# Performance work log

Measured on AMD Instinct MI355X. Metric: run time of the kernel, lower is better.

## Reference

```python
import jax, jax.numpy as jnp
import numpy as np

BS, N, DIM, HEADS = 4, 2048, 512, 8
HEAD_DIM = DIM // HEADS
SCALE = HEAD_DIM ** 0.5
NEG = -1000000.0


def setup_inputs() -> dict:
    key = jax.random.key(0)
    ks = jax.random.split(key, 6)
    x = jax.random.normal(ks[0], (BS, N, DIM), dtype=jnp.float32)
    mask = jax.random.randint(ks[1], (BS, N), 0, 2, dtype=jnp.int32)
    s = 1.0 / np.sqrt(DIM)
    Wq = jax.random.normal(ks[2], (DIM, DIM), dtype=jnp.float32) * s
    Wk = jax.random.normal(ks[3], (DIM, DIM), dtype=jnp.float32) * s
    Wv = jax.random.normal(ks[4], (DIM, DIM), dtype=jnp.float32) * s
    Wo = jax.random.normal(ks[5], (DIM, DIM), dtype=jnp.float32) * s
    return {"x": x, "Wq": Wq, "Wk": Wk, "Wv": Wv, "Wo": Wo, "mask": mask}


def reference(x, Wq, Wk, Wv, Wo, mask):
    # q,k,v: (bs, n, dim) -> (bs, h, n, d)
    def split_heads(t):
        return t.reshape(BS, N, HEADS, HEAD_DIM).transpose(0, 2, 1, 3)
    q = split_heads(x @ Wq.T)
    k = split_heads(x @ Wk.T)
    v = split_heads(x @ Wv.T)
    # scores: (bs, h, n, n)
    scores = jnp.einsum('bhqd,bhkd->bhqk', q, k) / SCALE
    # key-padding mask broadcast over heads and query positions
    keep = (mask == 1)[:, None, None, :]  # (bs,1,1,n)
    scores = jnp.where(keep, scores, NEG)
    attn = jax.nn.softmax(scores, axis=-1)
    out = jnp.einsum('bhqk,bhkd->bhqd', attn, v)
    out = out.transpose(0, 2, 1, 3).reshape(BS, N, DIM)
    return out @ Wo.T
```

## Files before the change

kernel.cpp:

```cpp
#include <hip/hip_runtime.h>
#include <hip/hip_bf16.h>

#define BS 4
#define SEQ 2048
#define DIM 512
#define HEADS 8
#define HD 64
#define ROWS (BS*SEQ)
#define SCL2E 0.1803368801111244f
#define NEGB (-1.4426950408889634e6f)

typedef __attribute__((ext_vector_type(8))) short bf16x8;
typedef __attribute__((ext_vector_type(4))) short bf16x4;
typedef __attribute__((ext_vector_type(4))) float floatx4;
typedef unsigned short u16;
typedef unsigned int u32;

#if defined(__has_builtin)
# if __has_builtin(__builtin_amdgcn_mfma_f32_16x16x16bf16_1k)
#  define HAVE_MFMA16 1
# endif
#endif
#ifndef HAVE_MFMA16
# define HAVE_MFMA16 0
#endif

__device__ __forceinline__ u16 f2bf(float f) {
    union { float f; unsigned u; } v; v.f = f;
    unsigned r = v.u + 0x7fff + ((v.u >> 16) & 1);
    return (u16)(r >> 16);
}

__device__ __forceinline__ unsigned pack2bf(float a, float b) {
#if __has_builtin(__builtin_amdgcn_cvt_pk_bf16_f32)
    typedef __attribute__((ext_vector_type(2))) __bf16 bf2;
    union { bf2 v; unsigned u; } cv;
    cv.v = __builtin_amdgcn_cvt_pk_bf16_f32(a, b);
    return cv.u;
#else
    return (unsigned)f2bf(a) | ((unsigned)f2bf(b) << 16);
#endif
}

__device__ __forceinline__ float fexp2(float x) {
#if __has_builtin(__builtin_amdgcn_exp2f)
    return __builtin_amdgcn_exp2f(x);
#else
    return __expf(x * 0.6931471805599453f);
#endif
}

__device__ __forceinline__ void gload16(const u16* g, u16* l) {
    __builtin_amdgcn_global_load_lds(
        (const __attribute__((address_space(1))) u32*)g,
        (__attribute__((address_space(3))) u32*)l, 16, 0, 0);
}

__global__ __launch_bounds__(256) void convert_all(
    const float* __restrict__ x, const float* __restrict__ Wq,
    const float* __restrict__ Wk, const float* __restrict__ Wv,
    const float* __restrict__ Wo, const int* __restrict__ mask,
    u16* __restrict__ xb, u16* __restrict__ wqb,
    u16* __restrict__ wkb, u16* __restrict__ wvb,
    u16* __restrict__ wob, float* __restrict__ biasf)
{
    int i = blockIdx.x * 256 + threadIdx.x;
    if (i < 1048576 + 262144) {
        const float* src; u16* dst; int off;
        if (i < 1048576) { src = x; dst = xb; off = i; }
        else {
            int j = i - 1048576; int seg = j >> 16; off = j & 65535;
            src = seg == 0 ? Wq : seg == 1 ? Wk : seg == 2 ? Wv : Wo;
            dst = seg == 0 ? wqb : seg == 1 ? wkb : seg == 2 ? wvb : wob;
        }
        float4 v = ((const float4*)src)[off];
        ushort4 o;
        o.x = f2bf(v.x); o.y = f2bf(v.y); o.z = f2bf(v.z); o.w = f2bf(v.w);
        ((ushort4*)dst)[off] = o;
    } else {
        int jb = i - 1310720;
        int4 mv = ((const int4*)mask)[jb];
        float4 bo;
        bo.x = (mv.x == 1) ? 0.f : NEGB;
        bo.y = (mv.y == 1) ? 0.f : NEGB;
        bo.z = (mv.z == 1) ? 0.f : NEGB;
        bo.w = (mv.w == 1) ? 0.f : NEGB;
        ((float4*)biasf)[jb] = bo;
    }
}

__global__ __launch_bounds__(256, 3) void gemm_qkv_fused(
    const u16* __restrict__ A, const u16* __restrict__ Wcat,
    u16* __restrict__ Oq, u16* __restrict__ Okf, u16* __restrict__ Ovf)
{
    __shared__ u16 ldsA[8192];
    __shared__ u16 ldsB[8192];

    int n0 = blockIdx.x * 128;
    int m0 = blockIdx.y * 128;
    int tid = threadIdx.x;
    int w = tid >> 6, lane = tid & 63, quad = lane >> 4, l16 = lane & 15;
    int mo = (w & 1) * 64, no = (w >> 1) * 64;
    int l7 = l16 & 7;

    int sr = lane >> 3, sc = lane & 7, gc = sc ^ sr;
    const u16* gA0 = A    + (long)(m0 + sr) * DIM + gc * 8;
    const u16* gB0 = Wcat + (long)(n0 + sr) * DIM + gc * 8;

    floatx4 acc[4][4];
    #pragma unroll
    for (int mt = 0; mt < 4; mt++)
        #pragma unroll
        for (int nt = 0; nt < 4; nt++) acc[mt][nt] = (floatx4){0.f,0.f,0.f,0.f};

    for (int k0 = 0; k0 < DIM; k0 += 64) {
        #pragma unroll
        for (int i = 0; i < 4; i++) {
            int ch = w * 4 + i;
            gload16(gA0 + (long)ch * 8 * DIM + k0, &ldsA[ch * 512]);
            gload16(gB0 + (long)ch * 8 * DIM + k0, &ldsB[ch * 512]);
        }
        __syncthreads();

        #pragma unroll
        for (int kc = 0; kc < 2; kc++) {
            int swz = ((kc * 4 + quad) ^ l7) * 8;
            bf16x8 af[4], bf[4];
            #pragma unroll
            for (int t4 = 0; t4 < 4; t4++) {
                af[t4] = *(const bf16x8*)&ldsA[(mo + t4*16 + l16) * 64 + swz];
                bf[t4] = *(const bf16x8*)&ldsB[(no + t4*16 + l16) * 64 + swz];
            }
            #pragma unroll
            for (int mt = 0; mt < 4; mt++)
                #pragma unroll
                for (int nt = 0; nt < 4; nt++)
                    acc[mt][nt] = __builtin_amdgcn_mfma_f32_16x16x32_bf16(
                        af[mt], bf[nt], acc[mt][nt], 0, 0, 0);
        }
        __syncthreads();
    }

    int seg = n0 >> 9;
    if (seg == 0) {
        #pragma unroll
        for (int mt = 0; mt < 4; mt++)
            #pragma unroll
            for (int nt = 0; nt < 4; nt++)
                #pragma unroll
                for (int r = 0; r < 4; r++) {
                    int row = m0 + mo + mt*16 + quad*4 + r;
                    int col9 = (n0 + no + nt*16 + l16) & 511;
                    int b = row >> 11, n = row & 2047, h = col9 >> 6, d = col9 & 63;
                    Oq[(((long)(b * HEADS + h) * SEQ + n) << 6) + d] = f2bf(acc[mt][nt][r]);
                }
    } else if (seg == 1) {
        #pragma unroll
        for (int mt = 0; mt < 4; mt++)
            #pragma unroll
            for (int nt = 0; nt < 4; nt++)
                #pragma unroll
                for (int r = 0; r < 4; r++) {
                    int row = m0 + mo + mt*16 + quad*4 + r;
                    int col9 = (n0 + no + nt*16 + l16) & 511;
                    int b = row >> 11, keyn = row & 2047, h = col9 >> 6, dd = col9 & 63;
                    int kt = keyn >> 6, ntk = (keyn >> 4) & 3, l16k = keyn & 15;
                    int g = dd >> 5, quadk = (dd >> 3) & 3, j = dd & 7;
                    long offv = ((long)((b*HEADS + h)*32 + kt) << 12)
                              + ((ntk*2 + g) << 9) + ((quadk*16 + l16k) << 3) + j;
                    Okf[offv] = f2bf(acc[mt][nt][r] * SCL2E);
                }
    } else {
#if HAVE_MFMA16
        #pragma unroll
        for (int mt = 0; mt < 4; mt++)
            #pragma unroll
            for (int nt = 0; nt < 4; nt++) {
                int rowb = m0 + mo + mt*16 + quad*4;
                int col9 = (n0 + no + nt*16 + l16) & 511;
                int b = rowb >> 11, keyn = rowb & 2047, h = col9 >> 6, dd = col9 & 63;
                int kt = keyn >> 6;
                int klo16 = mt;
                int ctv = dd >> 4, d15 = dd & 15;
                long offv = ((long)((b*HEADS + h)*32 + kt) << 12)
                          + ((klo16*4 + ctv) << 8) + ((quad*16 + d15) << 2);
                ushort4 st;
                st.x = f2bf(acc[mt][nt][0]); st.y = f2bf(acc[mt][nt][1]);
                st.z = f2bf(acc[mt][nt][2]); st.w = f2bf(acc[mt][nt][3]);
                *(ushort4*)&Ovf[offv] = st;
            }
#else
        #pragma unroll
        for (int mt = 0; mt < 4; mt++)
            #pragma unroll
            for (int nt = 0; nt < 4; nt++) {
                int rowb = m0 + mo + mt*16 + quad*4;
                int col9 = (n0 + no + nt*16 + l16) & 511;
                int b = rowb >> 11, keyn = rowb & 2047, h = col9 >> 6, dd = col9 & 63;
                int kt = keyn >> 6, g = (keyn >> 5) & 1, quadv = (keyn >> 3) & 3, jk = keyn & 7;
                int ctv = dd >> 4, l16v = dd & 15;
                long offv = ((long)((b*HEADS + h)*32 + kt) << 12)
                          + ((ctv*2 + g) << 9) + ((quadv*16 + l16v) << 3) + jk;
                ushort4 st;
                st.x = f2bf(acc[mt][nt][0]); st.y = f2bf(acc[mt][nt][1]);
                st.z = f2bf(acc[mt][nt][2]); st.w = f2bf(acc[mt][nt][3]);
                *(ushort4*)&Ovf[offv] = st;
            }
#endif
    }
}

#if HAVE_MFMA16
__global__ __launch_bounds__(256, 3) void flash_attn(
    const u16* __restrict__ Q, const u16* __restrict__ Kf,
    const u16* __restrict__ Vf, const float* __restrict__ biasf,
    u16* __restrict__ ctx)
{
    __shared__ u16 lds[16384];

    int bx = blockIdx.x;
    int q0 = (bx & 31) * 64;
    int h  = (bx >> 5) & 7;
    int b  = bx >> 8;
    int bh = b * HEADS + h;

    int tid = threadIdx.x;
    int w = tid >> 6, lane = tid & 63, quad = lane >> 4, l16 = lane & 15;

    bf16x8 qb[4][2];
    #pragma unroll
    for (int nt = 0; nt < 4; nt++) {
        const u16* qp = Q + ((long)bh * SEQ + q0 + nt*16 + l16) * HD + quad * 8;
        qb[nt][0] = *(const bf16x8*)(qp);
        qb[nt][1] = *(const bf16x8*)(qp + 32);
    }

    const u16* Kbh = Kf + ((long)bh << 17);
    const u16* Vbh = Vf + ((long)bh << 17);
    const float* bb = biasf + b * SEQ + w*16 + quad*4;

    u16* K0 = &lds[0];    u16* K1 = &lds[4096];
    u16* V0 = &lds[8192]; u16* V1 = &lds[12288];

    gload16(Kbh + w*1024       + lane*8, K0 + w*1024);
    gload16(Kbh + w*1024 + 512 + lane*8, K0 + w*1024 + 512);
    gload16(Vbh + w*1024       + lane*8, V0 + w*1024);
    gload16(Vbh + w*1024 + 512 + lane*8, V0 + w*1024 + 512);

    floatx4 o[4][4];
    #pragma unroll
    for (int nt = 0; nt < 4; nt++)
        #pragma unroll
        for (int ct = 0; ct < 4; ct++) o[nt][ct] = (floatx4){0.f,0.f,0.f,0.f};
    float ls[4] = {0.f, 0.f, 0.f, 0.f};

    for (int t = 0; t < 32; t++) {
        u16* Kc = (t & 1) ? K1 : K0;
        u16* Vc = (t & 1) ? V1 : V0;
        u16* Kn = (t & 1) ? K0 : K1;
        u16* Vn = (t & 1) ? V0 : V1;

        __builtin_amdgcn_s_waitcnt(0x0F70);

        bf16x8 ka0 = *(const bf16x8*)(Kc + w*1024       + lane*8);
        bf16x8 ka1 = *(const bf16x8*)(Kc + w*1024 + 512 + lane*8);
        bf16x4 vb[4];
        #pragma unroll
        for (int ct = 0; ct < 4; ct++)
            vb[ct] = *(const bf16x4*)(Vc + w*1024 + ct*256 + lane*4);

        if (t < 31) {
            const u16* kp = Kbh + (long)(t+1)*4096 + w*1024 + lane*8;
            const u16* vp = Vbh + (long)(t+1)*4096 + w*1024 + lane*8;
            gload16(kp,       Kn + w*1024);
            gload16(kp + 512, Kn + w*1024 + 512);
            gload16(vp,       Vn + w*1024);
            gload16(vp + 512, Vn + w*1024 + 512);
        }

        float4 bv = *(const float4*)(bb + t*64);

        #pragma unroll
        for (int nt = 0; nt < 4; nt++) {
            floatx4 s;
            s[0] = bv.x; s[1] = bv.y; s[2] = bv.z; s[3] = bv.w;
            s = __builtin_amdgcn_mfma_f32_16x16x32_bf16(ka0, qb[nt][0], s, 0, 0, 0);
            s = __builtin_amdgcn_mfma_f32_16x16x32_bf16(ka1, qb[nt][1], s, 0, 0, 0);
            float p0 = fexp2(s[0]);
            float p1 = fexp2(s[1]);
            float p2 = fexp2(s[2]);
            float p3 = fexp2(s[3]);
            ls[nt] += (p0 + p1) + (p2 + p3);
            union { bf16x4 v; unsigned u[2]; } pu;
            pu.u[0] = pack2bf(p0, p1);
            pu.u[1] = pack2bf(p2, p3);
            #pragma unroll
            for (int ct = 0; ct < 4; ct++)
                o[nt][ct] = __builtin_amdgcn_mfma_f32_16x16x16bf16_1k(
                    pu.v, vb[ct], o[nt][ct], 0, 0, 0);
        }
    }

    __syncthreads();
    float* ldsf = (float*)lds;
    floatx4* ldsv = (floatx4*)lds;

    #pragma unroll
    for (int nt = 0; nt < 4; nt++) {
        ls[nt] += __shfl_xor(ls[nt], 16);
        ls[nt] += __shfl_xor(ls[nt], 32);
    }
    if (quad == 0) {
        #pragma unroll
        for (int nt = 0; nt < 4; nt++)
            ldsf[4096 + w*64 + nt*16 + l16] = ls[nt];
    }
    __syncthreads();

    #pragma unroll
    for (int i = 1; i < 4; i++) {
        int tslot = (w + i) & 3;
        #pragma unroll
        for (int nt = 0; nt < 4; nt++)
            if (nt == tslot) {
                #pragma unroll
                for (int ct = 0; ct < 4; ct++)
                    ldsv[nt*256 + ct*64 + lane] = o[nt][ct];
            }
        __syncthreads();
        #pragma unroll
        for (int nt = 0; nt < 4; nt++)
            if (nt == w) {
                #pragma unroll
                for (int ct = 0; ct < 4; ct++) {
                    floatx4 v = ldsv[nt*256 + ct*64 + lane];
                    o[nt][ct] += v;
                }
            }
        __syncthreads();
    }

    #pragma unroll
    for (int nt = 0; nt < 4; nt++) {
        if (nt != w) continue;
        float inv[4];
        #pragma unroll
        for (int r = 0; r < 4; r++) {
            int q = w*16 + quad*4 + r;
            float s = ldsf[4096 + q] + ldsf[4096 + 64 + q]
                    + ldsf[4096 + 128 + q] + ldsf[4096 + 192 + q];
            inv[r] = 1.0f / s;
        }
        #pragma unroll
        for (int ct = 0; ct < 4; ct++) {
            int col = h * HD + ct*16 + l16;
            long rb = (long)(b * SEQ + q0 + w*16 + quad*4);
            #pragma unroll
            for (int r = 0; r < 4; r++)
                ctx[(rb + r) * DIM + col] = f2bf(o[nt][ct][r] * inv[r]);
        }
    }
}
#else
__global__ __launch_bounds__(256, 4) void flash_attn(
    const u16* __restrict__ Q, const u16* __restrict__ Kf,
    const u16* __restrict__ Vf, const float* __restrict__ biasf,
    u16* __restrict__ ctx)
{
    __shared__ u16 lds[20480];

    int bx = blockIdx.x;
    int q0 = (bx & 31) * 64;
    int h  = (bx >> 5) & 7;
    int b  = bx >> 8;
    int bh = b * HEADS + h;

    int tid = threadIdx.x;
    int w = tid >> 6, lane = tid & 63, quad = lane >> 4, l16 = lane & 15;

    const u16* Qp = Q + ((long)bh * SEQ + q0 + w*16 + l16) * HD + quad * 8;
    bf16x8 qb0 = *(const bf16x8*)(Qp);
    bf16x8 qb1 = *(const bf16x8*)(Qp + 32);

    const u16* Kbh = Kf + ((long)bh << 17);
    const u16* Vbh = Vf + ((long)bh << 17);
    const float* bbase = biasf + b * SEQ + quad * 4;

    u16* Prow = &lds[16384 + w * 1024 + l16 * 64];
    int swz = l16 & 7;

    {
        const u16* gk = Kbh + (2*w)*512 + lane*8;
        const u16* gv = Vbh + (2*w)*512 + lane*8;
        gload16(gk,       &lds[(2*w)*512]);
        gload16(gk + 512, &lds[(2*w+1)*512]);
        gload16(gv,       &lds[8192 + (2*w)*512]);
        gload16(gv + 512, &lds[8192 + (2*w+1)*512]);
    }
    __syncthreads();

    floatx4 o[4];
    #pragma unroll
    for (int ct = 0; ct < 4; ct++) o[ct] = (floatx4){0.f, 0.f, 0.f, 0.f};
    float lsum = 0.f;

    for (int t = 0; t < 32; t++) {
        int cur = t & 1;
        if (t < 31) {
            long tb = (long)(t + 1) << 12;
            int nb = cur ^ 1;
            const u16* gk = Kbh + tb + (2*w)*512 + lane*8;
            const u16* gv = Vbh + tb + (2*w)*512 + lane*8;
            gload16(gk,       &lds[nb*4096 + (2*w)*512]);
            gload16(gk + 512, &lds[nb*4096 + (2*w+1)*512]);
            gload16(gv,       &lds[8192 + nb*4096 + (2*w)*512]);
            gload16(gv + 512, &lds[8192 + nb*4096 + (2*w+1)*512]);
        }

        const u16* Kl = &lds[cur * 4096];
        const u16* Vl = &lds[8192 + cur * 4096];

        #pragma unroll
        for (int nt = 0; nt < 4; nt++) {
            float4 bv = *(const float4*)(bbase + t*64 + nt*16);
            bf16x8 ka0 = *(const bf16x8*)(Kl + (nt*2 + 0)*512 + lane*8);
            bf16x8 ka1 = *(const bf16x8*)(Kl + (nt*2 + 1)*512 + lane*8);
            floatx4 tt;
            tt[0] = bv.x; tt[1] = bv.y; tt[2] = bv.z; tt[3] = bv.w;
            tt = __builtin_amdgcn_mfma_f32_16x16x32_bf16(ka0, qb0, tt, 0, 0, 0);
            tt = __builtin_amdgcn_mfma_f32_16x16x32_bf16(ka1, qb1, tt, 0, 0, 0);
            float p0 = fexp2(tt[0]);
            float p1 = fexp2(tt[1]);
            float p2 = fexp2(tt[2]);
            float p3 = fexp2(tt[3]);
            lsum += (p0 + p1) + (p2 + p3);
            int gx = nt*2 + (quad >> 1);
            uint2 pu;
            pu.x = pack2bf(p0, p1);
            pu.y = pack2bf(p2, p3);
            *(uint2*)(Prow + ((gx ^ swz) << 3) + (quad & 1)*4) = pu;
        }

        #pragma unroll
        for (int g = 0; g < 2; g++) {
            bf16x8 pa = *(const bf16x8*)(Prow + (((g*4 + quad) ^ swz) << 3));
            #pragma unroll
            for (int ct = 0; ct < 4; ct++) {
                bf16x8 vbf = *(const bf16x8*)(Vl + (ct*2 + g)*512 + lane*8);
                o[ct] = __builtin_amdgcn_mfma_f32_16x16x32_bf16(pa, vbf, o[ct], 0, 0, 0);
            }
        }

        __syncthreads();
    }

    lsum += __shfl_xor(lsum, 16);
    lsum += __shfl_xor(lsum, 32);
    float inv = 1.0f / lsum;
    float i0 = __shfl(inv, quad*4 + 0);
    float i1 = __shfl(inv, quad*4 + 1);
    float i2 = __shfl(inv, quad*4 + 2);
    float i3 = __shfl(inv, quad*4 + 3);
    #pragma unroll
    for (int ct = 0; ct < 4; ct++) {
        int col = h * HD + ct*16 + l16;
        long rb = (long)(b * SEQ + q0 + w*16 + quad*4);
        ctx[(rb + 0) * DIM + col] = f2bf(o[ct][0] * i0);
        ctx[(rb + 1) * DIM + col] = f2bf(o[ct][1] * i1);
        ctx[(rb + 2) * DIM + col] = f2bf(o[ct][2] * i2);
        ctx[(rb + 3) * DIM + col] = f2bf(o[ct][3] * i3);
    }
}
#endif

__global__ __launch_bounds__(256, 3) void gemm_proj(
    const u16* __restrict__ A, const u16* __restrict__ Bt,
    float* __restrict__ Out)
{
    __shared__ u16 ldsA[8192];
    __shared__ u16 ldsB[8192];

    int n0 = blockIdx.x * 128;
    int m0 = blockIdx.y * 128;
    int tid = threadIdx.x;
    int w = tid >> 6, lane = tid & 63, quad = lane >> 4, l16 = lane & 15;
    int mo = (w & 1) * 64, no = (w >> 1) * 64;
    int l7 = l16 & 7;

    int sr = lane >> 3, sc = lane & 7, gc = sc ^ sr;
    const u16* gA0 = A  + (long)(m0 + sr) * DIM + gc * 8;
    const u16* gB0 = Bt + (long)(n0 + sr) * DIM + gc * 8;

    floatx4 acc[4][4];
    #pragma unroll
    for (int mt = 0; mt < 4; mt++)
        #pragma unroll
        for (int nt = 0; nt < 4; nt++) acc[mt][nt] = (floatx4){0.f,0.f,0.f,0.f};

    for (int k0 = 0; k0 < DIM; k0 += 64) {
        #pragma unroll
        for (int i = 0; i < 4; i++) {
            int ch = w * 4 + i;
            gload16(gA0 + (long)ch * 8 * DIM + k0, &ldsA[ch * 512]);
            gload16(gB0 + (long)ch * 8 * DIM + k0, &ldsB[ch * 512]);
        }
        __syncthreads();

        #pragma unroll
        for (int kc = 0; kc < 2; kc++) {
            int swz = ((kc * 4 + quad) ^ l7) * 8;
            bf16x8 af[4], bf[4];
            #pragma unroll
            for (int t4 = 0; t4 < 4; t4++) {
                af[t4] = *(const bf16x8*)&ldsA[(mo + t4*16 + l16) * 64 + swz];
                bf[t4] = *(const bf16x8*)&ldsB[(no + t4*16 + l16) * 64 + swz];
            }
            #pragma unroll
            for (int mt = 0; mt < 4; mt++)
                #pragma unroll
                for (int nt = 0; nt < 4; nt++)
                    acc[mt][nt] = __builtin_amdgcn_mfma_f32_16x16x32_bf16(
                        af[mt], bf[nt], acc[mt][nt], 0, 0, 0);
        }
        __syncthreads();
    }

    #pragma unroll
    for (int mt = 0; mt < 4; mt++)
        #pragma unroll
        for (int nt = 0; nt < 4; nt++)
            #pragma unroll
            for (int r = 0; r < 4; r++) {
                int row = m0 + mo + mt*16 + quad*4 + r;
                int col = n0 + no + nt*16 + l16;
                Out[(long)row * DIM + col] = acc[mt][nt][r];
            }
}

extern "C" void kernel_launch(void* const* d_in, const int* in_sizes, int n_in,
                              void* d_out, int out_size, void* d_ws, size_t ws_size,
                              hipStream_t stream) {
    const float* x  = (const float*)d_in[0];
    const float* Wq = (const float*)d_in[1];
    const float* Wk = (const float*)d_in[2];
    const float* Wv = (const float*)d_in[3];
    const float* Wo = (const float*)d_in[4];
    const int* mask = (const int*)d_in[5];
    float* out = (float*)d_out;

    char* ws = (char*)d_ws;
    size_t off = 0;
    u16* xb  = (u16*)(ws + off); off += (size_t)ROWS * DIM * 2;
    u16* wqb = (u16*)(ws + off); off += (size_t)DIM * DIM * 2;
    u16* wkb = (u16*)(ws + off); off += (size_t)DIM * DIM * 2;
    u16* wvb = (u16*)(ws + off); off += (size_t)DIM * DIM * 2;
    u16* wob = (u16*)(ws + off); off += (size_t)DIM * DIM * 2;
    u16* Qh  = (u16*)(ws + off); off += (size_t)ROWS * DIM * 2;
    u16* Kfr = (u16*)(ws + off); off += (size_t)ROWS * DIM * 2;
    u16* Vfr = (u16*)(ws + off); off += (size_t)ROWS * DIM * 2;
    u16* ctx = (u16*)(ws + off); off += (size_t)ROWS * DIM * 2;
    float* biasf = (float*)(ws + off); off += (size_t)BS * SEQ * 4;

    convert_all<<<5128, 256, 0, stream>>>(x, Wq, Wk, Wv, Wo, mask,
                                          xb, wqb, wkb, wvb, wob, biasf);
    gemm_qkv_fused<<<dim3(12, 64), 256, 0, stream>>>(xb, wqb, Qh, Kfr, Vfr);
    flash_attn<<<BS * HEADS * (SEQ / 64), 256, 0, stream>>>(Qh, Kfr, Vfr, biasf, ctx);
    gemm_proj<<<dim3(4, 64), 256, 0, stream>>>(ctx, wob, out);

    (void)in_sizes; (void)n_in; (void)out_size; (void)ws_size;
}
```

Before: 173.5 us.

## Load K/V fragments directly to registers in attention and shrink projection tiles

Measured after the change: 164.3 us. 5.3% less time.

```diff
diff --git a/kernel.cpp b/kernel.cpp
--- a/kernel.cpp
+++ b/kernel.cpp
@@ -180,10 +180,10 @@
                 int col9 = (n0 + no + nt*16 + l16) & 511;
                 int b = rowb >> 11, keyn = rowb & 2047, h = col9 >> 6, dd = col9 & 63;
                 int kt = keyn >> 6;
-                int klo16 = mt;
-                int ctv = dd >> 4, d15 = dd & 15;
+                int wf = (keyn >> 4) & 3, quadf = (keyn >> 2) & 3;
+                int ctf = dd >> 4, l16f = dd & 15;
                 long offv = ((long)((b*HEADS + h)*32 + kt) << 12)
-                          + ((klo16*4 + ctv) << 8) + ((quad*16 + d15) << 2);
+                          + (wf << 10) + ((quadf*16 + l16f) << 4) + (ctf << 2);
                 ushort4 st;
                 st.x = f2bf(acc[mt][nt][0]); st.y = f2bf(acc[mt][nt][1]);
                 st.z = f2bf(acc[mt][nt][2]); st.w = f2bf(acc[mt][nt][3]);
@@ -216,7 +216,7 @@
     const u16* __restrict__ Vf, const float* __restrict__ biasf,
     u16* __restrict__ ctx)
 {
-    __shared__ u16 lds[16384];
+    __shared__ float red[4352];
 
     int bx = blockIdx.x;
     int q0 = (bx & 31) * 64;
@@ -235,17 +235,15 @@
         qb[nt][1] = *(const bf16x8*)(qp + 32);
     }
 
-    const u16* Kbh = Kf + ((long)bh << 17);
-    const u16* Vbh = Vf + ((long)bh << 17);
+    const u16* Kbh = Kf + ((long)bh << 17) + w*1024 + lane*8;
+    const u16* Vbh = Vf + ((long)bh << 17) + w*1024 + lane*16;
     const float* bb = biasf + b * SEQ + w*16 + quad*4;
 
-    u16* K0 = &lds[0];    u16* K1 = &lds[4096];
-    u16* V0 = &lds[8192]; u16* V1 = &lds[12288];
-
-    gload16(Kbh + w*1024       + lane*8, K0 + w*1024);
-    gload16(Kbh + w*1024 + 512 + lane*8, K0 + w*1024 + 512);
-    gload16(Vbh + w*1024       + lane*8, V0 + w*1024);
-    gload16(Vbh + w*1024 + 512 + lane*8, V0 + w*1024 + 512);
+    bf16x8 ka0 = *(const bf16x8*)(Kbh);
+    bf16x8 ka1 = *(const bf16x8*)(Kbh + 512);
+    bf16x8 vlo = *(const bf16x8*)(Vbh);
+    bf16x8 vhi = *(const bf16x8*)(Vbh + 8);
+    float4 bv  = *(const float4*)(bb);
 
     floatx4 o[4][4];
     #pragma unroll
@@ -254,31 +252,23 @@
         for (int ct = 0; ct < 4; ct++) o[nt][ct] = (floatx4){0.f,0.f,0.f,0.f};
     float ls[4] = {0.f, 0.f, 0.f, 0.f};
 
+    #pragma unroll 2
     for (int t = 0; t < 32; t++) {
-        u16* Kc = (t & 1) ? K1 : K0;
-        u16* Vc = (t & 1) ? V1 : V0;
-        u16* Kn = (t & 1) ? K0 : K1;
-        u16* Vn = (t & 1) ? V0 : V1;
-
-        __builtin_amdgcn_s_waitcnt(0x0F70);
-
-        bf16x8 ka0 = *(const bf16x8*)(Kc + w*1024       + lane*8);
-        bf16x8 ka1 = *(const bf16x8*)(Kc + w*1024 + 512 + lane*8);
-        bf16x4 vb[4];
-        #pragma unroll
-        for (int ct = 0; ct < 4; ct++)
-            vb[ct] = *(const bf16x4*)(Vc + w*1024 + ct*256 + lane*4);
-
+        bf16x8 ka0n = ka0, ka1n = ka1, vlon = vlo, vhin = vhi;
+        float4 bvn = bv;
         if (t < 31) {
-            const u16* kp = Kbh + (long)(t+1)*4096 + w*1024 + lane*8;
-            const u16* vp = Vbh + (long)(t+1)*4096 + w*1024 + lane*8;
-            gload16(kp,       Kn + w*1024);
-            gload16(kp + 512, Kn + w*1024 + 512);
-            gload16(vp,       Vn + w*1024);
-            gload16(vp + 512, Vn + w*1024 + 512);
-        }
-
-        float4 bv = *(const float4*)(bb + t*64);
+            const u16* kp = Kbh + (long)(t+1)*4096;
+            const u16* vp = Vbh + (long)(t+1)*4096;
+            ka0n = *(const bf16x8*)(kp);
+            ka1n = *(const bf16x8*)(kp + 512);
+            vlon = *(const bf16x8*)(vp);
+            vhin = *(const bf16x8*)(vp + 8);
+            bvn  = *(const float4*)(bb + (t+1)*64);
+        }
+
+        union { bf16x8 v8; bf16x4 v4[2]; } uvl, uvh;
+        uvl.v8 = vlo; uvh.v8 = vhi;
+        bf16x4 vb[4] = { uvl.v4[0], uvl.v4[1], uvh.v4[0], uvh.v4[1] };
 
         #pragma unroll
         for (int nt = 0; nt < 4; nt++) {
@@ -299,11 +289,13 @@
                 o[nt][ct] = __builtin_amdgcn_mfma_f32_16x16x16bf16_1k(
                     pu.v, vb[ct], o[nt][ct], 0, 0, 0);
         }
+
+        ka0 = ka0n; ka1 = ka1n; vlo = vlon; vhi = vhin; bv = bvn;
     }
 
     __syncthreads();
-    float* ldsf = (float*)lds;
-    floatx4* ldsv = (floatx4*)lds;
+    float* ldsf = red;
+    floatx4* ldsv = (floatx4*)red;
 
     #pragma unroll
     for (int nt = 0; nt < 4; nt++) {
@@ -473,68 +465,57 @@
 }
 #endif
 
-__global__ __launch_bounds__(256, 3) void gemm_proj(
+__global__ __launch_bounds__(256, 4) void gemm_proj(
     const u16* __restrict__ A, const u16* __restrict__ Bt,
     float* __restrict__ Out)
 {
-    __shared__ u16 ldsA[8192];
+    __shared__ u16 ldsA[4096];
     __shared__ u16 ldsB[8192];
 
     int n0 = blockIdx.x * 128;
-    int m0 = blockIdx.y * 128;
+    int m0 = blockIdx.y * 64;
     int tid = threadIdx.x;
     int w = tid >> 6, lane = tid & 63, quad = lane >> 4, l16 = lane & 15;
-    int mo = (w & 1) * 64, no = (w >> 1) * 64;
     int l7 = l16 & 7;
 
     int sr = lane >> 3, sc = lane & 7, gc = sc ^ sr;
     const u16* gA0 = A  + (long)(m0 + sr) * DIM + gc * 8;
     const u16* gB0 = Bt + (long)(n0 + sr) * DIM + gc * 8;
 
-    floatx4 acc[4][4];
-    #pragma unroll
-    for (int mt = 0; mt < 4; mt++)
-        #pragma unroll
-        for (int nt = 0; nt < 4; nt++) acc[mt][nt] = (floatx4){0.f,0.f,0.f,0.f};
+    floatx4 acc[8];
+    #pragma unroll
+    for (int nt = 0; nt < 8; nt++) acc[nt] = (floatx4){0.f,0.f,0.f,0.f};
 
     for (int k0 = 0; k0 < DIM; k0 += 64) {
-        #pragma unroll
-        for (int i = 0; i < 4; i++) {
-            int ch = w * 4 + i;
-            gload16(gA0 + (long)ch * 8 * DIM + k0, &ldsA[ch * 512]);
-            gload16(gB0 + (long)ch * 8 * DIM + k0, &ldsB[ch * 512]);
-        }
+        gload16(gA0 + (long)(2*w)   * 8 * DIM + k0, &ldsA[(2*w)   * 512]);
+        gload16(gA0 + (long)(2*w+1) * 8 * DIM + k0, &ldsA[(2*w+1) * 512]);
+        #pragma unroll
+        for (int i = 0; i < 4; i++)
+            gload16(gB0 + (long)(4*w+i) * 8 * DIM + k0, &ldsB[(4*w+i) * 512]);
         __syncthreads();
 
         #pragma unroll
         for (int kc = 0; kc < 2; kc++) {
             int swz = ((kc * 4 + quad) ^ l7) * 8;
-            bf16x8 af[4], bf[4];
-            #pragma unroll
-            for (int t4 = 0; t4 < 4; t4++) {
-                af[t4] = *(const bf16x8*)&ldsA[(mo + t4*16 + l16) * 64 + swz];
-                bf[t4] = *(const bf16x8*)&ldsB[(no + t4*16 + l16) * 64 + swz];
-            }
-            #pragma unroll
-            for (int mt = 0; mt < 4; mt++)
-                #pragma unroll
-                for (int nt = 0; nt < 4; nt++)
-                    acc[mt][nt] = __builtin_amdgcn_mfma_f32_16x16x32_bf16(
-                        af[mt], bf[nt], acc[mt][nt], 0, 0, 0);
-        }
-        __syncthreads();
-    }
-
-    #pragma unroll
-    for (int mt = 0; mt < 4; mt++)
-        #pragma unroll
-        for (int nt = 0; nt < 4; nt++)
-            #pragma unroll
-            for (int r = 0; r < 4; r++) {
-                int row = m0 + mo + mt*16 + quad*4 + r;
-                int col = n0 + no + nt*16 + l16;
-                Out[(long)row * DIM + col] = acc[mt][nt][r];
-            }
+            bf16x8 af = *(const bf16x8*)&ldsA[(w*16 + l16) * 64 + swz];
+            #pragma unroll
+            for (int nt = 0; nt < 8; nt++) {
+                bf16x8 bfv = *(const bf16x8*)&ldsB[(nt*16 + l16) * 64 + swz];
+                acc[nt] = __builtin_amdgcn_mfma_f32_16x16x32_bf16(
+                    af, bfv, acc[nt], 0, 0, 0);
+            }
+        }
+        __syncthreads();
+    }
+
+    #pragma unroll
+    for (int nt = 0; nt < 8; nt++)
+        #pragma unroll
+        for (int r = 0; r < 4; r++) {
+            int row = m0 + w*16 + quad*4 + r;
+            int col = n0 + nt*16 + l16;
+            Out[(long)row * DIM + col] = acc[nt][r];
+        }
 }
 
 extern "C" void kernel_launch(void* const* d_in, const int* in_sizes, int n_in,
@@ -565,7 +546,7 @@
                                           xb, wqb, wkb, wvb, wob, biasf);
     gemm_qkv_fused<<<dim3(12, 64), 256, 0, stream>>>(xb, wqb, Qh, Kfr, Vfr);
     flash_attn<<<BS * HEADS * (SEQ / 64), 256, 0, stream>>>(Qh, Kfr, Vfr, biasf, ctx);
-    gemm_proj<<<dim3(4, 64), 256, 0, stream>>>(ctx, wob, out);
+    gemm_proj<<<dim3(4, 128), 256, 0, stream>>>(ctx, wob, out);
 
     (void)in_sizes; (void)n_in; (void)out_size; (void)ws_size;
 }
```
